# Kernel tuning notes

Measured on AMD Instinct MI355X. Metric: run time of the kernel, lower is better.

Reference implementation:

```python
import jax, jax.numpy as jnp
import numpy as np

EPS = 1e-5
DN = ('NCDHW', 'OIDHW', 'NCDHW')

def conv3d(x, w, b):
    y = jax.lax.conv_general_dilated(x, w, (1, 1, 1), 'SAME', dimension_numbers=DN)
    return y + b[None, :, None, None, None]

def batchnorm(x, gamma, beta):
    # training-mode BatchNorm3d: biased batch stats over (N, D, H, W) per channel
    mean = jnp.mean(x, axis=(0, 2, 3, 4), keepdims=True)
    var = jnp.mean((x - mean) ** 2, axis=(0, 2, 3, 4), keepdims=True)
    xhat = (x - mean) * jax.lax.rsqrt(var + EPS)
    return gamma[None, :, None, None, None] * xhat + beta[None, :, None, None, None]

def setup_inputs() -> dict:
    key = jax.random.key(0)
    ks = jax.random.split(key, 8)
    C, N = 32, 4  # channel, fuzzynum
    B, D, H, W = 4, 64, 64, 64
    x = jax.random.normal(ks[0], (B, C, D, H, W), dtype=jnp.float32)
    fan1 = C * 27
    conv1_w = jax.random.uniform(ks[1], (1, C, 3, 3, 3), jnp.float32, -1, 1) / np.sqrt(fan1)
    conv1_b = jnp.zeros((1,), jnp.float32)
    fan2 = 1 * 27
    conv2_w = jax.random.uniform(ks[2], (C, 1, 3, 3, 3), jnp.float32, -1, 1) / np.sqrt(fan2)
    conv2_b = jnp.zeros((C,), jnp.float32)
    mu = jax.random.normal(ks[3], (C, N), dtype=jnp.float32)
    sigma = jax.random.normal(ks[4], (C, N), dtype=jnp.float32)
    bn1_g = jnp.ones((1,), jnp.float32)
    bn1_b = jnp.zeros((1,), jnp.float32)
    bn2_g = jnp.ones((C,), jnp.float32)
    bn2_b = jnp.zeros((C,), jnp.float32)
    return {"x": x, "conv1_w": conv1_w, "conv1_b": conv1_b, "conv2_w": conv2_w,
            "conv2_b": conv2_b, "mu": mu, "sigma": sigma,
            "bn1_g": bn1_g, "bn1_b": bn1_b, "bn2_g": bn2_g, "bn2_b": bn2_b}

def reference(x, conv1_w, conv1_b, conv2_w, conv2_b, mu, sigma, bn1_g, bn1_b, bn2_g, bn2_b):
    x1 = conv3d(x, conv1_w, conv1_b)                      # [B,1,D,H,W]
    # fuzzy Gaussian membership: only channel 0 of mu/sigma is used (x1 has 1 channel)
    m = mu[0]                                             # [n]
    s = sigma[0]                                          # [n]
    z = (x1[..., None] - m) / s                           # [B,1,D,H,W,n]
    fuzz = jnp.exp(-jnp.sum(z * z, axis=-1))              # [B,1,D,H,W]
    y = batchnorm(fuzz, bn1_g, bn1_b)
    y = conv3d(y, conv2_w, conv2_b)                       # [B,C,D,H,W]
    return batchnorm(y, bn2_g, bn2_b)
```

## Files before the change

kernel.cpp:

```cpp
#include <hip/hip_runtime.h>

constexpr int Cc = 32;
constexpr int SP = 64 * 64 * 64;
constexpr int TS = 4 * SP;


__global__ __launch_bounds__(256) void k_conv1_fuzzy(
    const float* __restrict__ x, const float* __restrict__ w1,
    const float* __restrict__ b1, const float* __restrict__ mu,
    const float* __restrict__ sg, float* __restrict__ fuzz,
    float* __restrict__ acc)
{
    const int tid = threadIdx.x;
    const int t = blockIdx.x * 256 + tid;
    const int wq = t & 15;        const int w0 = wq << 2;
    const int zp = (t >> 4) & 31; const int z0 = zp << 1;
    const int y  = (t >> 9) & 63;
    const int b  = t >> 15;
    const int lane = tid & 63;

    float S1 = 0.f, S2 = 0.f, S3 = 0.f;
#pragma unroll
    for (int n = 0; n < 4; n++) {
        float m = mu[n], s = sg[n];
        float iv = 1.0f / (s * s);
        S1 += iv; S2 += m * iv; S3 += m * m * iv;
    }

    const float b1v = b1[0];
    float a00 = b1v, a01 = b1v, a02 = b1v, a03 = b1v;
    float a10 = b1v, a11 = b1v, a12 = b1v, a13 = b1v;

    const float* xb = x + (size_t)b * Cc * SP;

    bool pv[12]; int ofs[12];
#pragma unroll
    for (int rz = 0; rz < 4; rz++) {
        const int zz = z0 - 1 + rz;
        const bool okz = (unsigned)zz < 64u;
#pragma unroll
        for (int dy = 0; dy < 3; dy++) {
            const int yy = y - 1 + dy;
            pv[rz * 3 + dy]  = okz && ((unsigned)yy < 64u);
            ofs[rz * 3 + dy] = (zz << 12) + (yy << 6) + w0;
        }
    }

    auto LOADCH = [&](int c, float4 (&M)[12]) {
        const float* xc = xb + (size_t)c * SP;
#pragma unroll
        for (int i = 0; i < 12; i++)
            M[i] = pv[i] ? *(const float4*)(xc + ofs[i])
                         : make_float4(0.f, 0.f, 0.f, 0.f);
    };

    auto COMPUTECH = [&](int c, const float4 (&M)[12]) {
        const float* wc = w1 + c * 27;
        float Wv[27];
#pragma unroll
        for (int k = 0; k < 27; k++) Wv[k] = wc[k];
#pragma unroll
        for (int rz = 0; rz < 4; rz++) {
#pragma unroll
            for (int dy = 0; dy < 3; dy++) {
                const float4 m = M[rz * 3 + dy];
                const float lv = __shfl(m.w, (lane + 63) & 63, 64);
                const float rv = __shfl(m.x, (lane + 1) & 63, 64);
                const float v0 = (wq > 0)  ? lv : 0.f;
                const float v5 = (wq < 15) ? rv : 0.f;
                const float v1 = m.x, v2 = m.y, v3 = m.z, v4 = m.w;
                if (rz < 3) {
                    const float W0 = Wv[(rz*3+dy)*3], W1 = Wv[(rz*3+dy)*3+1], W2 = Wv[(rz*3+dy)*3+2];
                    a00 = fmaf(v0, W0, fmaf(v1, W1, fmaf(v2, W2, a00)));
                    a01 = fmaf(v1, W0, fmaf(v2, W1, fmaf(v3, W2, a01)));
                    a02 = fmaf(v2, W0, fmaf(v3, W1, fmaf(v4, W2, a02)));
                    a03 = fmaf(v3, W0, fmaf(v4, W1, fmaf(v5, W2, a03)));
                }
                if (rz >= 1) {
                    const float W0 = Wv[((rz-1)*3+dy)*3], W1 = Wv[((rz-1)*3+dy)*3+1], W2 = Wv[((rz-1)*3+dy)*3+2];
                    a10 = fmaf(v0, W0, fmaf(v1, W1, fmaf(v2, W2, a10)));
                    a11 = fmaf(v1, W0, fmaf(v2, W1, fmaf(v3, W2, a11)));
                    a12 = fmaf(v2, W0, fmaf(v3, W1, fmaf(v4, W2, a12)));
                    a13 = fmaf(v3, W0, fmaf(v4, W1, fmaf(v5, W2, a13)));
                }
            }
        }
    };

    float4 Ma[12], Mb[12];
    LOADCH(0, Ma);
    for (int c = 0; c < Cc; c += 2) {
        LOADCH(c + 1, Mb);
        COMPUTECH(c, Ma);
        if (c + 2 < Cc) LOADCH(c + 2, Ma);
        COMPUTECH(c + 1, Mb);
    }

    float fsum = 0.f, fsq = 0.f;
#pragma unroll
    for (int oz = 0; oz < 2; oz++) {
        float xv[4] = { oz ? a10 : a00, oz ? a11 : a01,
                        oz ? a12 : a02, oz ? a13 : a03 };
        float4 fv; float* fp = &fv.x;
#pragma unroll
        for (int ow = 0; ow < 4; ow++) {
            float x1 = xv[ow];
            float tt = x1 * x1 * S1 - 2.0f * x1 * S2 + S3;
            float fz = __expf(-tt);
            fp[ow] = fz; fsum += fz; fsq += fz * fz;
        }
        *(float4*)(fuzz + (size_t)b * SP + ((z0 + oz) << 12) + (y << 6) + w0) = fv;
    }
#pragma unroll
    for (int m = 1; m < 64; m <<= 1) {
        fsum += __shfl_xor(fsum, m, 64);
        fsq  += __shfl_xor(fsq,  m, 64);
    }
    __shared__ float red[8];
    const int wid = tid >> 6;
    if ((tid & 63) == 0) { red[wid * 2] = fsum; red[wid * 2 + 1] = fsq; }
    __syncthreads();
    if (tid == 0) {
        atomicAdd(&acc[0], red[0] + red[2] + red[4] + red[6]);
        atomicAdd(&acc[1], red[1] + red[3] + red[5] + red[7]);
    }
}

__global__ void k_fin1(const float* __restrict__ g, const float* __restrict__ be,
                       float* __restrict__ acc)
{
    float mean = acc[0] * (1.0f / TS);
    float var  = acc[1] * (1.0f / TS) - mean * mean;
    float a = g[0] * rsqrtf(var + 1e-5f);
    acc[2] = a;
    acc[3] = be[0] - mean * a;
}

__global__ __launch_bounds__(256) void k_conv2_stats(
    const float* __restrict__ fuzz, const float* __restrict__ w2,
    const float* __restrict__ b2, float* __restrict__ acc)
{
    const int tid = threadIdx.x;
    const int t = blockIdx.x * 256 + tid;
    const int lane = tid & 63;
    const int w = t & 63;
    const int y = (t >> 6) & 63;
    const int z0 = ((t >> 12) & 15) << 2;
    const int b = t >> 16;
    const float a = acc[2], sh = acc[3];
    const float* fb = fuzz + (size_t)b * SP;

    float Fl[6][3], Fm[6][3], Fr[6][3];
#pragma unroll
    for (int rz = 0; rz < 6; rz++) {
        const int zz = z0 - 1 + rz;
        const bool okz = (unsigned)zz < 64u;
#pragma unroll
        for (int dy = 0; dy < 3; dy++) {
            const int yy = y - 1 + dy;
            float f = 0.f;
            if (okz && (unsigned)yy < 64u)
                f = fmaf(a, fb[(zz << 12) + (yy << 6) + w], sh);
            const float lv = __shfl(f, (lane + 63) & 63, 64);
            const float rv = __shfl(f, (lane + 1) & 63, 64);
            Fm[rz][dy] = f;
            Fl[rz][dy] = (w > 0)  ? lv : 0.f;
            Fr[rz][dy] = (w < 63) ? rv : 0.f;
        }
    }

    __shared__ float red[2][32][4];
    const int wid = tid >> 6;

#pragma unroll
    for (int c = 0; c < Cc; c++) {
        const float* wc = w2 + c * 27;
        float Wv[27];
#pragma unroll
        for (int k = 0; k < 27; k++) Wv[k] = wc[k];
        const float bb = b2[c];
        float o0 = bb, o1 = bb, o2 = bb, o3 = bb;
#pragma unroll
        for (int rz = 0; rz < 6; rz++) {
#pragma unroll
            for (int dy = 0; dy < 3; dy++) {
                const float l = Fl[rz][dy], m = Fm[rz][dy], r = Fr[rz][dy];
#pragma unroll
                for (int oz = 0; oz < 4; oz++) {
                    const int dz = rz - oz;
                    if (dz < 0 || dz > 2) continue;
                    const float W0 = Wv[(dz*3+dy)*3], W1 = Wv[(dz*3+dy)*3+1], W2 = Wv[(dz*3+dy)*3+2];
                    if      (oz == 0) o0 = fmaf(l, W0, fmaf(m, W1, fmaf(r, W2, o0)));
                    else if (oz == 1) o1 = fmaf(l, W0, fmaf(m, W1, fmaf(r, W2, o1)));
                    else if (oz == 2) o2 = fmaf(l, W0, fmaf(m, W1, fmaf(r, W2, o2)));
                    else              o3 = fmaf(l, W0, fmaf(m, W1, fmaf(r, W2, o3)));
                }
            }
        }
        float ps = (o0 + o1) + (o2 + o3);
        float pq = fmaf(o0, o0, fmaf(o1, o1, fmaf(o2, o2, o3 * o3)));
#pragma unroll
        for (int mm = 1; mm < 64; mm <<= 1) {
            ps += __shfl_xor(ps, mm, 64);
            pq += __shfl_xor(pq, mm, 64);
        }
        if (lane == 0) { red[0][c][wid] = ps; red[1][c][wid] = pq; }
    }
    __syncthreads();
    if (tid < 64) {
        const int c = tid & 31, st = tid >> 5;
        const float v = red[st][c][0] + red[st][c][1] + red[st][c][2] + red[st][c][3];
        atomicAdd(&acc[4 + st * 32 + c], v);
    }
}

__global__ void k_fin2(const float* __restrict__ g, const float* __restrict__ be,
                       float* __restrict__ acc)
{
    int c = threadIdx.x;
    float mean = acc[4 + c] * (1.0f / TS);
    float var  = acc[36 + c] * (1.0f / TS) - mean * mean;
    float sc = g[c] * rsqrtf(var + 1e-5f);
    acc[68 + c]  = sc;
    acc[100 + c] = be[c] - mean * sc;
}

__global__ __launch_bounds__(256) void k_conv2_write(
    const float* __restrict__ fuzz, const float* __restrict__ w2,
    const float* __restrict__ b2, const float* __restrict__ acc,
    float* __restrict__ out)
{
    const int tid = threadIdx.x;
    const int t = blockIdx.x * 256 + tid;
    const int lane = tid & 63;
    const int w = t & 63;
    const int y = (t >> 6) & 63;
    const int z0 = ((t >> 12) & 31) << 1;
    const int b = t >> 17;
    const float a = acc[2], sh = acc[3];
    const float* fb = fuzz + (size_t)b * SP;

    float Fl[4][3], Fm[4][3], Fr[4][3];
#pragma unroll
    for (int rz = 0; rz < 4; rz++) {
        const int zz = z0 - 1 + rz;
        const bool okz = (unsigned)zz < 64u;
#pragma unroll
        for (int dy = 0; dy < 3; dy++) {
            const int yy = y - 1 + dy;
            float f = 0.f;
            if (okz && (unsigned)yy < 64u)
                f = fmaf(a, fb[(zz << 12) + (yy << 6) + w], sh);
            const float lv = __shfl(f, (lane + 63) & 63, 64);
            const float rv = __shfl(f, (lane + 1) & 63, 64);
            Fm[rz][dy] = f;
            Fl[rz][dy] = (w > 0)  ? lv : 0.f;
            Fr[rz][dy] = (w < 63) ? rv : 0.f;
        }
    }

    float* ob = out + (size_t)b * Cc * SP + (z0 << 12) + (y << 6) + w;
#pragma unroll
    for (int c = 0; c < Cc; c++) {
        const float* wc = w2 + c * 27;
        float Wv[27];
#pragma unroll
        for (int k = 0; k < 27; k++) Wv[k] = wc[k];
        const float bb = b2[c];
        float o0 = bb, o1 = bb;
#pragma unroll
        for (int rz = 0; rz < 4; rz++) {
#pragma unroll
            for (int dy = 0; dy < 3; dy++) {
                const float l = Fl[rz][dy], m = Fm[rz][dy], r = Fr[rz][dy];
#pragma unroll
                for (int oz = 0; oz < 2; oz++) {
                    const int dz = rz - oz;
                    if (dz < 0 || dz > 2) continue;
                    const float W0 = Wv[(dz*3+dy)*3], W1 = Wv[(dz*3+dy)*3+1], W2 = Wv[(dz*3+dy)*3+2];
                    if (oz == 0) o0 = fmaf(l, W0, fmaf(m, W1, fmaf(r, W2, o0)));
                    else         o1 = fmaf(l, W0, fmaf(m, W1, fmaf(r, W2, o1)));
                }
            }
        }
        const float sc = acc[68 + c], shf = acc[100 + c];
        ob[(size_t)c * SP]        = fmaf(o0, sc, shf);
        ob[(size_t)c * SP + 4096] = fmaf(o1, sc, shf);
    }
}

extern "C" void kernel_launch(void* const* d_in, const int* in_sizes, int n_in,
                              void* d_out, int out_size, void* d_ws, size_t ws_size,
                              hipStream_t stream)
{
    const float* x   = (const float*)d_in[0];
    const float* w1  = (const float*)d_in[1];
    const float* b1  = (const float*)d_in[2];
    const float* w2  = (const float*)d_in[3];
    const float* b2  = (const float*)d_in[4];
    const float* mu  = (const float*)d_in[5];
    const float* sg  = (const float*)d_in[6];
    const float* g1  = (const float*)d_in[7];
    const float* be1 = (const float*)d_in[8];
    const float* g2  = (const float*)d_in[9];
    const float* be2 = (const float*)d_in[10];

    float* out  = (float*)d_out;
    float* fuzz = (float*)d_ws;
    float* acc  = fuzz + TS;

    hipMemsetAsync(acc, 0, 132 * sizeof(float), stream);
    k_conv1_fuzzy<<<512, 256, 0, stream>>>(x, w1, b1, mu, sg, fuzz, acc);
    k_fin1<<<1, 1, 0, stream>>>(g1, be1, acc);
    k_conv2_stats<<<1024, 256, 0, stream>>>(fuzz, w2, b2, acc);
    k_fin2<<<1, 32, 0, stream>>>(g2, be2, acc);
    k_conv2_write<<<2048, 256, 0, stream>>>(fuzz, w2, b2, acc, out);
}
```

Measured before the change: 411.0 us.

## Store raw conv2 output once, apply BN2 in-place pass, shrink conv1 tile

Conv2 was computed twice, once for statistics and again for the normalized write. Now a single fused kernel writes the raw conv2 output and accumulates per-channel statistics into 64 slots per channel to reduce atomic contention, and a separate elementwise kernel applies BN2 in place. Conv1 now computes one z-plane per thread instead of two, doubling the block count but reloading more input rows. The change trades the duplicate conv2 compute for an extra read and write pass over the 128MB output.

```diff
diff --git a/kernel.cpp b/kernel.cpp
--- a/kernel.cpp
+++ b/kernel.cpp
@@ -4,6 +4,7 @@
 constexpr int SP = 64 * 64 * 64;
 constexpr int TS = 4 * SP;
 
+constexpr int ACC_N = 68 + 64 * 64;
 
 __global__ __launch_bounds__(256) void k_conv1_fuzzy(
     const float* __restrict__ x, const float* __restrict__ w1,
@@ -14,9 +15,9 @@
     const int tid = threadIdx.x;
     const int t = blockIdx.x * 256 + tid;
     const int wq = t & 15;        const int w0 = wq << 2;
-    const int zp = (t >> 4) & 31; const int z0 = zp << 1;
-    const int y  = (t >> 9) & 63;
-    const int b  = t >> 15;
+    const int z  = (t >> 4) & 63;
+    const int y  = (t >> 10) & 63;
+    const int b  = t >> 16;
     const int lane = tid & 63;
 
     float S1 = 0.f, S2 = 0.f, S3 = 0.f;
@@ -28,15 +29,14 @@
     }
 
     const float b1v = b1[0];
-    float a00 = b1v, a01 = b1v, a02 = b1v, a03 = b1v;
-    float a10 = b1v, a11 = b1v, a12 = b1v, a13 = b1v;
+    float a0 = b1v, a1 = b1v, a2 = b1v, a3 = b1v;
 
     const float* xb = x + (size_t)b * Cc * SP;
 
-    bool pv[12]; int ofs[12];
-#pragma unroll
-    for (int rz = 0; rz < 4; rz++) {
-        const int zz = z0 - 1 + rz;
+    bool pv[9]; int ofs[9];
+#pragma unroll
+    for (int rz = 0; rz < 3; rz++) {
+        const int zz = z - 1 + rz;
         const bool okz = (unsigned)zz < 64u;
 #pragma unroll
         for (int dy = 0; dy < 3; dy++) {
@@ -46,48 +46,35 @@
         }
     }
 
-    auto LOADCH = [&](int c, float4 (&M)[12]) {
+    auto LOADCH = [&](int c, float4 (&M)[9]) {
         const float* xc = xb + (size_t)c * SP;
 #pragma unroll
-        for (int i = 0; i < 12; i++)
+        for (int i = 0; i < 9; i++)
             M[i] = pv[i] ? *(const float4*)(xc + ofs[i])
                          : make_float4(0.f, 0.f, 0.f, 0.f);
     };
 
-    auto COMPUTECH = [&](int c, const float4 (&M)[12]) {
+    auto COMPUTECH = [&](int c, const float4 (&M)[9]) {
         const float* wc = w1 + c * 27;
         float Wv[27];
 #pragma unroll
         for (int k = 0; k < 27; k++) Wv[k] = wc[k];
 #pragma unroll
-        for (int rz = 0; rz < 4; rz++) {
-#pragma unroll
-            for (int dy = 0; dy < 3; dy++) {
-                const float4 m = M[rz * 3 + dy];
-                const float lv = __shfl(m.w, (lane + 63) & 63, 64);
-                const float rv = __shfl(m.x, (lane + 1) & 63, 64);
-                const float v0 = (wq > 0)  ? lv : 0.f;
-                const float v5 = (wq < 15) ? rv : 0.f;
-                const float v1 = m.x, v2 = m.y, v3 = m.z, v4 = m.w;
-                if (rz < 3) {
-                    const float W0 = Wv[(rz*3+dy)*3], W1 = Wv[(rz*3+dy)*3+1], W2 = Wv[(rz*3+dy)*3+2];
-                    a00 = fmaf(v0, W0, fmaf(v1, W1, fmaf(v2, W2, a00)));
-                    a01 = fmaf(v1, W0, fmaf(v2, W1, fmaf(v3, W2, a01)));
-                    a02 = fmaf(v2, W0, fmaf(v3, W1, fmaf(v4, W2, a02)));
-                    a03 = fmaf(v3, W0, fmaf(v4, W1, fmaf(v5, W2, a03)));
-                }
-                if (rz >= 1) {
-                    const float W0 = Wv[((rz-1)*3+dy)*3], W1 = Wv[((rz-1)*3+dy)*3+1], W2 = Wv[((rz-1)*3+dy)*3+2];
-                    a10 = fmaf(v0, W0, fmaf(v1, W1, fmaf(v2, W2, a10)));
-                    a11 = fmaf(v1, W0, fmaf(v2, W1, fmaf(v3, W2, a11)));
-                    a12 = fmaf(v2, W0, fmaf(v3, W1, fmaf(v4, W2, a12)));
-                    a13 = fmaf(v3, W0, fmaf(v4, W1, fmaf(v5, W2, a13)));
-                }
-            }
+        for (int i = 0; i < 9; i++) {
+            const float4 m = M[i];
+            const float lv = __shfl(m.w, (lane + 63) & 63, 64);
+            const float rv = __shfl(m.x, (lane + 1) & 63, 64);
+            const float v0 = (wq > 0)  ? lv : 0.f;
+            const float v5 = (wq < 15) ? rv : 0.f;
+            const float W0 = Wv[i * 3], W1 = Wv[i * 3 + 1], W2 = Wv[i * 3 + 2];
+            a0 = fmaf(v0,  W0, fmaf(m.x, W1, fmaf(m.y, W2, a0)));
+            a1 = fmaf(m.x, W0, fmaf(m.y, W1, fmaf(m.z, W2, a1)));
+            a2 = fmaf(m.y, W0, fmaf(m.z, W1, fmaf(m.w, W2, a2)));
+            a3 = fmaf(m.z, W0, fmaf(m.w, W1, fmaf(v5,  W2, a3)));
         }
     };
 
-    float4 Ma[12], Mb[12];
+    float4 Ma[9], Mb[9];
     LOADCH(0, Ma);
     for (int c = 0; c < Cc; c += 2) {
         LOADCH(c + 1, Mb);
@@ -97,20 +84,17 @@
     }
 
     float fsum = 0.f, fsq = 0.f;
-#pragma unroll
-    for (int oz = 0; oz < 2; oz++) {
-        float xv[4] = { oz ? a10 : a00, oz ? a11 : a01,
-                        oz ? a12 : a02, oz ? a13 : a03 };
-        float4 fv; float* fp = &fv.x;
-#pragma unroll
-        for (int ow = 0; ow < 4; ow++) {
-            float x1 = xv[ow];
-            float tt = x1 * x1 * S1 - 2.0f * x1 * S2 + S3;
-            float fz = __expf(-tt);
-            fp[ow] = fz; fsum += fz; fsq += fz * fz;
-        }
-        *(float4*)(fuzz + (size_t)b * SP + ((z0 + oz) << 12) + (y << 6) + w0) = fv;
-    }
+    float xv[4] = { a0, a1, a2, a3 };
+    float4 fv; float* fp = &fv.x;
+#pragma unroll
+    for (int ow = 0; ow < 4; ow++) {
+        float x1 = xv[ow];
+        float tt = x1 * x1 * S1 - 2.0f * x1 * S2 + S3;
+        float fz = __expf(-tt);
+        fp[ow] = fz; fsum += fz; fsq += fz * fz;
+    }
+    *(float4*)(fuzz + (size_t)b * SP + (z << 12) + (y << 6) + w0) = fv;
+
 #pragma unroll
     for (int m = 1; m < 64; m <<= 1) {
         fsum += __shfl_xor(fsum, m, 64);
@@ -136,17 +120,19 @@
     acc[3] = be[0] - mean * a;
 }
 
-__global__ __launch_bounds__(256) void k_conv2_stats(
+__global__ __launch_bounds__(256) void k_conv2_fused(
     const float* __restrict__ fuzz, const float* __restrict__ w2,
-    const float* __restrict__ b2, float* __restrict__ acc)
+    const float* __restrict__ b2, float* __restrict__ acc,
+    float* __restrict__ out)
 {
     const int tid = threadIdx.x;
-    const int t = blockIdx.x * 256 + tid;
     const int lane = tid & 63;
-    const int w = t & 63;
-    const int y = (t >> 6) & 63;
-    const int z0 = ((t >> 12) & 15) << 2;
-    const int b = t >> 16;
+    const int wid = tid >> 6;
+    const int bi = blockIdx.x;
+    const int w = lane;
+    const int y = bi & 63;
+    const int z0 = ((bi >> 6) & 15) << 2;
+    const int b = bi >> 10;
     const float a = acc[2], sh = acc[3];
     const float* fb = fuzz + (size_t)b * SP;
 
@@ -169,11 +155,13 @@
         }
     }
 
-    __shared__ float red[2][32][4];
-    const int wid = tid >> 6;
-
-#pragma unroll
-    for (int c = 0; c < Cc; c++) {
+    float* ob = out + (size_t)b * Cc * SP + (z0 << 12) + (y << 6) + w;
+    const int slot = bi & 63;
+    const int c0 = wid * 8;
+
+#pragma unroll
+    for (int ci = 0; ci < 8; ci++) {
+        const int c = c0 + ci;
         const float* wc = w2 + c * 27;
         float Wv[27];
 #pragma unroll
@@ -197,6 +185,11 @@
                 }
             }
         }
+        ob[(size_t)c * SP]         = o0;
+        ob[(size_t)c * SP + 4096]  = o1;
+        ob[(size_t)c * SP + 8192]  = o2;
+        ob[(size_t)c * SP + 12288] = o3;
+
         float ps = (o0 + o1) + (o2 + o3);
         float pq = fmaf(o0, o0, fmaf(o1, o1, fmaf(o2, o2, o3 * o3)));
 #pragma unroll
@@ -204,13 +197,10 @@
             ps += __shfl_xor(ps, mm, 64);
             pq += __shfl_xor(pq, mm, 64);
         }
-        if (lane == 0) { red[0][c][wid] = ps; red[1][c][wid] = pq; }
-    }
-    __syncthreads();
-    if (tid < 64) {
-        const int c = tid & 31, st = tid >> 5;
-        const float v = red[st][c][0] + red[st][c][1] + red[st][c][2] + red[st][c][3];
-        atomicAdd(&acc[4 + st * 32 + c], v);
+        if (lane == 0) {
+            atomicAdd(&acc[68 + c * 64 + slot], ps);
+            atomicAdd(&acc[68 + (32 + c) * 64 + slot], pq);
+        }
     }
 }
 
@@ -218,75 +208,30 @@
                        float* __restrict__ acc)
 {
     int c = threadIdx.x;
-    float mean = acc[4 + c] * (1.0f / TS);
-    float var  = acc[36 + c] * (1.0f / TS) - mean * mean;
+    float s = 0.f, q = 0.f;
+    for (int k = 0; k < 64; k++) {
+        s += acc[68 + c * 64 + k];
+        q += acc[68 + (32 + c) * 64 + k];
+    }
+    float mean = s * (1.0f / TS);
+    float var  = q * (1.0f / TS) - mean * mean;
     float sc = g[c] * rsqrtf(var + 1e-5f);
-    acc[68 + c]  = sc;
-    acc[100 + c] = be[c] - mean * sc;
-}
-
-__global__ __launch_bounds__(256) void k_conv2_write(
-    const float* __restrict__ fuzz, const float* __restrict__ w2,
-    const float* __restrict__ b2, const float* __restrict__ acc,
-    float* __restrict__ out)
-{
-    const int tid = threadIdx.x;
-    const int t = blockIdx.x * 256 + tid;
-    const int lane = tid & 63;
-    const int w = t & 63;
-    const int y = (t >> 6) & 63;
-    const int z0 = ((t >> 12) & 31) << 1;
-    const int b = t >> 17;
-    const float a = acc[2], sh = acc[3];
-    const float* fb = fuzz + (size_t)b * SP;
-
-    float Fl[4][3], Fm[4][3], Fr[4][3];
-#pragma unroll
-    for (int rz = 0; rz < 4; rz++) {
-        const int zz = z0 - 1 + rz;
-        const bool okz = (unsigned)zz < 64u;
-#pragma unroll
-        for (int dy = 0; dy < 3; dy++) {
-            const int yy = y - 1 + dy;
-            float f = 0.f;
-            if (okz && (unsigned)yy < 64u)
-                f = fmaf(a, fb[(zz << 12) + (yy << 6) + w], sh);
-            const float lv = __shfl(f, (lane + 63) & 63, 64);
-            const float rv = __shfl(f, (lane + 1) & 63, 64);
-            Fm[rz][dy] = f;
-            Fl[rz][dy] = (w > 0)  ? lv : 0.f;
-            Fr[rz][dy] = (w < 63) ? rv : 0.f;
-        }
-    }
-
-    float* ob = out + (size_t)b * Cc * SP + (z0 << 12) + (y << 6) + w;
-#pragma unroll
-    for (int c = 0; c < Cc; c++) {
-        const float* wc = w2 + c * 27;
-        float Wv[27];
-#pragma unroll
-        for (int k = 0; k < 27; k++) Wv[k] = wc[k];
-        const float bb = b2[c];
-        float o0 = bb, o1 = bb;
-#pragma unroll
-        for (int rz = 0; rz < 4; rz++) {
-#pragma unroll
-            for (int dy = 0; dy < 3; dy++) {
-                const float l = Fl[rz][dy], m = Fm[rz][dy], r = Fr[rz][dy];
-#pragma unroll
-                for (int oz = 0; oz < 2; oz++) {
-                    const int dz = rz - oz;
-                    if (dz < 0 || dz > 2) continue;
-                    const float W0 = Wv[(dz*3+dy)*3], W1 = Wv[(dz*3+dy)*3+1], W2 = Wv[(dz*3+dy)*3+2];
-                    if (oz == 0) o0 = fmaf(l, W0, fmaf(m, W1, fmaf(r, W2, o0)));
-                    else         o1 = fmaf(l, W0, fmaf(m, W1, fmaf(r, W2, o1)));
-                }
-            }
-        }
-        const float sc = acc[68 + c], shf = acc[100 + c];
-        ob[(size_t)c * SP]        = fmaf(o0, sc, shf);
-        ob[(size_t)c * SP + 4096] = fmaf(o1, sc, shf);
-    }
+    acc[4 + c]  = sc;
+    acc[36 + c] = be[c] - mean * sc;
+}
+
+__global__ __launch_bounds__(256) void k_bn2_apply(
+    const float* __restrict__ acc, float* __restrict__ out)
+{
+    const int t = blockIdx.x * 256 + threadIdx.x;
+    const int c = (t >> 16) & 31;
+    const float sc = acc[4 + c], sh = acc[36 + c];
+    float4 v = ((const float4*)out)[t];
+    v.x = fmaf(v.x, sc, sh);
+    v.y = fmaf(v.y, sc, sh);
+    v.z = fmaf(v.z, sc, sh);
+    v.w = fmaf(v.w, sc, sh);
+    ((float4*)out)[t] = v;
 }
 
 extern "C" void kernel_launch(void* const* d_in, const int* in_sizes, int n_in,
@@ -309,10 +254,10 @@
     float* fuzz = (float*)d_ws;
     float* acc  = fuzz + TS;
 
-    hipMemsetAsync(acc, 0, 132 * sizeof(float), stream);
-    k_conv1_fuzzy<<<512, 256, 0, stream>>>(x, w1, b1, mu, sg, fuzz, acc);
+    hipMemsetAsync(acc, 0, ACC_N * sizeof(float), stream);
+    k_conv1_fuzzy<<<1024, 256, 0, stream>>>(x, w1, b1, mu, sg, fuzz, acc);
     k_fin1<<<1, 1, 0, stream>>>(g1, be1, acc);
-    k_conv2_stats<<<1024, 256, 0, stream>>>(fuzz, w2, b2, acc);
+    k_conv2_fused<<<4096, 256, 0, stream>>>(fuzz, w2, b2, acc, out);
     k_fin2<<<1, 32, 0, stream>>>(g2, be2, acc);
-    k_conv2_write<<<2048, 256, 0, stream>>>(fuzz, w2, b2, acc, out);
-}
+    k_bn2_apply<<<32768, 256, 0, stream>>>(acc, out);
+}
```

After: 462.8 us. 1.13x slower.
